# Optimization experiments

Measured on AMD Instinct MI355X. Metric: run time of the kernel, lower is better.

## Reference

```python
import jax, jax.numpy as jnp
import numpy as np

B, T, N, F = 32, 64, 256, 64
TOP_K = 0.2  # ratio of dims to keep per batch element


def setup_inputs() -> dict:
    key = jax.random.key(0)
    ks = jax.random.split(key, 12)
    w = lambda k, shape: jax.random.normal(k, shape, jnp.float32) * 0.05
    z = lambda: jnp.zeros((F,), jnp.float32)
    return {
        "x": jax.random.normal(ks[0], (B, T, N, F), jnp.float32),
        "Wc1": w(ks[1], (3, F, F)), "bc1": z(),
        "Wc2": w(ks[2], (3, F, F)), "bc2": z(),
        "Wc3": w(ks[3], (3, F, F)), "bc3": z(),
        "Wq": w(ks[4], (F, F)), "bq": z(),
        "Wk": w(ks[5], (F, F)), "bk": z(),
        "Wv": w(ks[6], (F, F)), "bv": z(),
        "Wd": w(ks[7], (F, F)), "bd": z(),
        "Wp": w(ks[8], (F, F)), "bp": z(),
    }


def _conv1d(x, W, b, dil):
    # x: [BN, T, F], W: [3, F, F] (WIO), dilated same-padded conv over time
    y = jax.lax.conv_general_dilated(
        x, W, window_strides=(1,), padding="SAME", rhs_dilation=(dil,),
        dimension_numbers=("NWC", "WIO", "NWC"))
    return y + b


@jax.custom_vjp
def ste_round(x):
    return jnp.round(x)

def _ste_fwd(x):
    return jnp.round(x), None

def _ste_bwd(res, g):
    # activation='linear': grad = upstream * 1
    return (g,)

ste_round.defvjp(_ste_fwd, _ste_bwd)


def reference(x, Wc1, bc1, Wc2, bc2, Wc3, bc3, Wq, bq, Wk, bk, Wv, bv, Wd, bd, Wp, bp):
    Bx, Tx, Nx, Fx = x.shape
    # --- dilated conv block over time axis (per node) ---
    xt = jnp.transpose(x, (0, 2, 1, 3)).reshape(Bx * Nx, Tx, Fx)  # [BN,T,F]
    c = jax.nn.relu(_conv1d(xt, Wc1, bc1, 1) + _conv1d(xt, Wc2, bc2, 2)
                    + _conv1d(xt, Wc3, bc3, 3))
    xt = xt + c
    x = jnp.transpose(xt.reshape(Bx, Nx, Tx, Fx), (0, 2, 1, 3))  # [B,T,N,F]
    # --- GAT attention over nodes (faithful: diagonal einsum 'btnn,btnf->btnf') ---
    Q = x @ Wq + bq
    K = x @ Wk + bk
    V = x @ Wv + bv
    scores = jnp.einsum("btnf,btmf->btnm", Q, K) / jnp.sqrt(jnp.float32(Fx))
    A = jax.nn.softmax(scores, axis=-1)
    g = jnp.einsum("btnn,btnf->btnf", A, V)  # diag(A) * V, as in the TF source
    x = x + jax.nn.relu(g)
    # --- dense projection ---
    x = x @ Wd + bd
    # --- inf-norm normalize over last axis, rescale to [0,1] ---
    norm = jnp.max(jnp.abs(x), axis=-1, keepdims=True)
    x = x / norm
    x = 0.5 * (x + 1.0)
    # --- per-batch top-k threshold via full sort ---
    n = Tx * Nx * Fx
    k = int(round(TOP_K * n))  # top_k < 1 => ratio, statically resolved
    ranking = jnp.sort(x.reshape(Bx, -1), axis=-1)  # ascending
    mu = ranking[:, -k - 1].reshape(Bx, 1, 1, 1)
    x = jax.nn.sigmoid(x - mu)
    # --- straight-through binary mask + frozen linear predictor ---
    mask = ste_round(x)
    masked = x * mask
    pred_on_masked = masked @ Wp + bp
    return pred_on_masked, mask
```

## Files before the change

### kernel.cpp

```cpp
#include <hip/hip_runtime.h>
#include <math.h>

#define BB 32
#define TT 64
#define NNODES 256
#define FDIM 64
#define SLICE (NNODES*FDIM)
#define NTOT (BB*TT*NNODES*FDIM)
#define RANK0 838860u

__global__ __launch_bounds__(256) void combine_w(
    const float* __restrict__ Wc1, const float* __restrict__ bc1,
    const float* __restrict__ Wc2, const float* __restrict__ bc2,
    const float* __restrict__ Wc3, const float* __restrict__ bc3,
    float* __restrict__ Wcomb, float* __restrict__ bcomb)
{
  const int FF2 = FDIM*FDIM;
  int gid = blockIdx.x*256 + threadIdx.x;
  if (gid < 7*FF2) {
    int j = gid / FF2, r = gid % FF2;
    float v;
    switch (j) {
      case 0: v = Wc3[r]; break;
      case 1: v = Wc2[r]; break;
      case 2: v = Wc1[r]; break;
      case 3: v = Wc1[FF2+r] + Wc2[FF2+r] + Wc3[FF2+r]; break;
      case 4: v = Wc1[2*FF2+r]; break;
      case 5: v = Wc2[2*FF2+r]; break;
      default: v = Wc3[2*FF2+r]; break;
    }
    Wcomb[gid] = v;
  }
  if (gid < FDIM) bcomb[gid] = bc1[gid] + bc2[gid] + bc3[gid];
}

__global__ __launch_bounds__(256,4) void conv_kernel(
    const float* __restrict__ x, const float* __restrict__ Wcomb,
    const float* __restrict__ bcomb, float* __restrict__ x1)
{
  __shared__ float xs[64*72];
  const int bn = blockIdx.x; const int b = bn >> 8; const int n = bn & 255;
  const int tid = threadIdx.x;
#pragma unroll
  for (int k=0;k<18;k++) xs[k*256+tid] = 0.f;
  __syncthreads();
  const float* xbase = x + ((size_t)b*TT)*SLICE + n*FDIM;
#pragma unroll
  for (int it=0; it<4; it++) {
    int flat4 = it*256 + tid;
    int t = flat4 >> 4, f4 = (flat4 & 15) << 2;
    float4 v = *(const float4*)(xbase + (size_t)t*SLICE + f4);
    xs[(f4+0)*72 + t+4] = v.x;
    xs[(f4+1)*72 + t+4] = v.y;
    xs[(f4+2)*72 + t+4] = v.z;
    xs[(f4+3)*72 + t+4] = v.w;
  }
  __syncthreads();
  const int o = tid & 63;
  const int tb = (tid >> 6) << 4;
  float acc[16];
  const float bco = bcomb[o];
#pragma unroll
  for (int k=0;k<16;k++) acc[k] = bco;
  for (int i=0;i<FDIM;i++) {
    float xr[24];
#pragma unroll
    for (int q=0;q<6;q++) {
      float4 v = *(const float4*)&xs[i*72 + tb + q*4];
      xr[q*4+0]=v.x; xr[q*4+1]=v.y; xr[q*4+2]=v.z; xr[q*4+3]=v.w;
    }
#pragma unroll
    for (int j=0;j<7;j++) {
      float w = Wcomb[(j*FDIM+i)*FDIM + o];
#pragma unroll
      for (int k=0;k<16;k++) acc[k] = fmaf(xr[k+j+1], w, acc[k]);
    }
  }
  float* obase = x1 + ((size_t)b*TT)*SLICE + n*FDIM + o;
#pragma unroll
  for (int k=0;k<16;k++) {
    int t = tb + k;
    float c = acc[k];
    float outv = xs[o*72 + t+4] + (c > 0.f ? c : 0.f);
    obase[(size_t)t*SLICE] = outv;
  }
}

__global__ __launch_bounds__(256,2) void attn_kernel(
    const float* __restrict__ x1,
    const float* __restrict__ Wq, const float* __restrict__ bq,
    const float* __restrict__ Wk, const float* __restrict__ bk,
    const float* __restrict__ Wv, const float* __restrict__ bv,
    const float* __restrict__ Wd, const float* __restrict__ bd,
    float* __restrict__ vout)
{
  __shared__ float ks[NNODES*68];
  const int bt = blockIdx.x;
  const int tid = threadIdx.x;
  const float4* xb4 = (const float4*)(x1 + (size_t)bt*SLICE);
#pragma unroll
  for (int it=0; it<16; it++) {
    int flat4 = it*256 + tid;
    int n = flat4 >> 4, f4 = (flat4 & 15) << 2;
    *(float4*)&ks[n*68 + f4] = xb4[flat4];
  }
  __syncthreads();
  float xr[64];
#pragma unroll
  for (int q=0;q<16;q++) {
    float4 v = *(const float4*)&ks[tid*68 + q*4];
    xr[q*4+0]=v.x; xr[q*4+1]=v.y; xr[q*4+2]=v.z; xr[q*4+3]=v.w;
  }
  {
    float a[64];
#pragma unroll
    for (int o=0;o<64;o++) a[o]=0.f;
    for (int i=0;i<64;i++) {
      float xv = xr[i];
#pragma unroll
      for (int o=0;o<64;o++) a[o] = fmaf(xv, Wk[i*64+o], a[o]);
    }
#pragma unroll
    for (int q=0;q<16;q++) {
      float4 w;
      w.x = a[q*4+0]+bk[q*4+0]; w.y = a[q*4+1]+bk[q*4+1];
      w.z = a[q*4+2]+bk[q*4+2]; w.w = a[q*4+3]+bk[q*4+3];
      *(float4*)&ks[tid*68 + q*4] = w;
    }
  }
  float qr[64];
#pragma unroll
  for (int o=0;o<64;o++) qr[o]=0.f;
  for (int i=0;i<64;i++) {
    float xv = xr[i];
#pragma unroll
    for (int o=0;o<64;o++) qr[o] = fmaf(xv, Wq[i*64+o], qr[o]);
  }
#pragma unroll
  for (int o=0;o<64;o++) qr[o] += bq[o];
  __syncthreads();
  float M = -3.402823466e38f, S = 0.f, diag = 0.f;
  for (int m=0;m<NNODES;m++) {
    float s = 0.f;
#pragma unroll
    for (int q=0;q<16;q++) {
      float4 kv = *(const float4*)&ks[m*68 + q*4];
      s = fmaf(qr[q*4+0], kv.x, s);
      s = fmaf(qr[q*4+1], kv.y, s);
      s = fmaf(qr[q*4+2], kv.z, s);
      s = fmaf(qr[q*4+3], kv.w, s);
    }
    s *= 0.125f;
    if (m == tid) diag = s;
    if (s > M) { S = S * expf(M - s) + 1.f; M = s; }
    else       { S += expf(s - M); }
  }
  const float ann = expf(diag - M) / S;
  float o1[64];
#pragma unroll
  for (int o=0;o<64;o++) o1[o]=0.f;
  for (int i=0;i<64;i++) {
    float xv = xr[i];
#pragma unroll
    for (int o=0;o<64;o++) o1[o] = fmaf(xv, Wv[i*64+o], o1[o]);
  }
#pragma unroll
  for (int o=0;o<64;o++) {
    float g = ann * (o1[o] + bv[o]);
    o1[o] = xr[o] + (g > 0.f ? g : 0.f);
  }
  float dd[64];
#pragma unroll
  for (int o=0;o<64;o++) dd[o]=0.f;
  for (int i=0;i<64;i++) {
    float ov = o1[i];
#pragma unroll
    for (int o=0;o<64;o++) dd[o] = fmaf(ov, Wd[i*64+o], dd[o]);
  }
  float nrm = 0.f;
#pragma unroll
  for (int o=0;o<64;o++) { dd[o] += bd[o]; nrm = fmaxf(nrm, fabsf(dd[o])); }
  __syncthreads();
#pragma unroll
  for (int q=0;q<16;q++) {
    float4 w;
    w.x = 0.5f*(dd[q*4+0]/nrm + 1.f);
    w.y = 0.5f*(dd[q*4+1]/nrm + 1.f);
    w.z = 0.5f*(dd[q*4+2]/nrm + 1.f);
    w.w = 0.5f*(dd[q*4+3]/nrm + 1.f);
    *(float4*)&ks[tid*68 + q*4] = w;
  }
  __syncthreads();
  float4* ob4 = (float4*)(vout + (size_t)bt*SLICE);
#pragma unroll
  for (int it=0;it<16;it++) {
    int flat4 = it*256 + tid;
    int n = flat4 >> 4, f4 = (flat4 & 15) << 2;
    ob4[flat4] = *(const float4*)&ks[n*68 + f4];
  }
}

template<int LEVEL>
__global__ __launch_bounds__(256) void hist_kernel(
    const float* __restrict__ v, unsigned* __restrict__ ghist,
    const unsigned* __restrict__ pfx)
{
  __shared__ unsigned h[4096];
  const int batch = blockIdx.x >> 5, chunk = blockIdx.x & 31;
  const int tid = threadIdx.x;
#pragma unroll
  for (int k=0;k<16;k++) h[k*256+tid] = 0u;
  __syncthreads();
  const unsigned p = pfx ? pfx[batch] : 0u;
  const float4* vb = (const float4*)(v + (size_t)batch*(TT*SLICE)) + chunk*8192 + tid;
  for (int k=0;k<32;k++) {
    float4 q = vb[k*256];
    float e[4] = {q.x,q.y,q.z,q.w};
#pragma unroll
    for (int j=0;j<4;j++) {
      unsigned u = __float_as_uint(e[j]);
      if (LEVEL==1) atomicAdd(&h[u>>20], 1u);
      else if ((u>>20)==p) atomicAdd(&h[(u>>8)&0xFFFu], 1u);
    }
  }
  __syncthreads();
  unsigned* gh = ghist + batch*4096;
#pragma unroll
  for (int k=0;k<16;k++) { unsigned c = h[k*256+tid]; if (c) atomicAdd(&gh[k*256+tid], c); }
}

__global__ __launch_bounds__(256) void hist8_kernel(
    const float* __restrict__ v, unsigned* __restrict__ ghist,
    const unsigned* __restrict__ pfx)
{
  __shared__ unsigned h[256];
  const int batch = blockIdx.x >> 5, chunk = blockIdx.x & 31;
  const int tid = threadIdx.x;
  h[tid] = 0u;
  __syncthreads();
  const unsigned p = pfx[batch];
  const float4* vb = (const float4*)(v + (size_t)batch*(TT*SLICE)) + chunk*8192 + tid;
  for (int k=0;k<32;k++) {
    float4 q = vb[k*256];
    float e[4] = {q.x,q.y,q.z,q.w};
#pragma unroll
    for (int j=0;j<4;j++) {
      unsigned u = __float_as_uint(e[j]);
      if ((u>>8)==p) atomicAdd(&h[u & 255u], 1u);
    }
  }
  __syncthreads();
  unsigned c = h[tid];
  if (c) atomicAdd(&ghist[batch*256+tid], c);
}

template<int PER>
__global__ __launch_bounds__(256) void find_kernel(
    const unsigned* __restrict__ hist,
    const unsigned* __restrict__ rank_in, const unsigned* __restrict__ pfx_in,
    int pfx_shift, unsigned* __restrict__ pfx_out, unsigned* __restrict__ rank_out,
    float* __restrict__ mu, int final_level)
{
  __shared__ unsigned csum[256];
  const int batch = blockIdx.x;
  const int tid = threadIdx.x;
  const unsigned* hb = hist + batch*(PER*256);
  unsigned loc[PER];
  unsigned s = 0;
#pragma unroll
  for (int q=0;q<PER;q++) { loc[q] = hb[tid*PER+q]; s += loc[q]; }
  csum[tid] = s;
  __syncthreads();
  for (int off=1; off<256; off<<=1) {
    unsigned vv = csum[tid];
    unsigned ad = (tid >= off) ? csum[tid-off] : 0u;
    __syncthreads();
    csum[tid] = vv + ad;
    __syncthreads();
  }
  const unsigned rank = rank_in ? rank_in[batch] : RANK0;
  const unsigned excl = csum[tid] - s;
  if (rank >= excl && rank < excl + s) {
    unsigned r = rank - excl;
    int bin = 0;
#pragma unroll
    for (int q=0;q<PER;q++) {
      if (r < loc[q]) { bin = tid*PER + q; break; }
      r -= loc[q];
    }
    unsigned pf = pfx_in ? pfx_in[batch] : 0u;
    unsigned np = (pf << pfx_shift) | (unsigned)bin;
    if (final_level) { mu[batch] = __uint_as_float(np); }
    else { pfx_out[batch] = np; rank_out[batch] = r; }
  }
}

__global__ __launch_bounds__(256,2) void final_kernel(
    const float* __restrict__ v, const float* __restrict__ mu,
    const float* __restrict__ Wp, const float* __restrict__ bp,
    float* __restrict__ pred, float* __restrict__ mask)
{
  __shared__ float sl[NNODES*68];
  const int bt = blockIdx.x;
  const int b = bt >> 6;
  const int tid = threadIdx.x;
  const float4* vb4 = (const float4*)(v + (size_t)bt*SLICE);
#pragma unroll
  for (int it=0; it<16; it++) {
    int flat4 = it*256 + tid;
    int n = flat4 >> 4, f4 = (flat4 & 15) << 2;
    *(float4*)&sl[n*68 + f4] = vb4[flat4];
  }
  __syncthreads();
  const float muv = mu[b];
  float srow[64];
#pragma unroll
  for (int q=0;q<16;q++) {
    float4 vv = *(const float4*)&sl[tid*68 + q*4];
    float e0 = 1.f/(1.f + expf(-(vv.x - muv)));
    float e1 = 1.f/(1.f + expf(-(vv.y - muv)));
    float e2 = 1.f/(1.f + expf(-(vv.z - muv)));
    float e3 = 1.f/(1.f + expf(-(vv.w - muv)));
    float m0 = rintf(e0), m1 = rintf(e1), m2 = rintf(e2), m3 = rintf(e3);
    srow[q*4+0] = e0*m0; srow[q*4+1] = e1*m1; srow[q*4+2] = e2*m2; srow[q*4+3] = e3*m3;
    float4 w; w.x=m0; w.y=m1; w.z=m2; w.w=m3;
    *(float4*)&sl[tid*68 + q*4] = w;
  }
  __syncthreads();
  float4* mb4 = (float4*)(mask + (size_t)bt*SLICE);
#pragma unroll
  for (int it=0; it<16; it++) {
    int flat4 = it*256 + tid;
    int n = flat4 >> 4, f4 = (flat4 & 15) << 2;
    mb4[flat4] = *(const float4*)&sl[n*68 + f4];
  }
  float acc[64];
#pragma unroll
  for (int o=0;o<64;o++) acc[o]=0.f;
  for (int i=0;i<64;i++) {
    float sv = srow[i];
#pragma unroll
    for (int o=0;o<64;o++) acc[o] = fmaf(sv, Wp[i*64+o], acc[o]);
  }
  __syncthreads();
#pragma unroll
  for (int q=0;q<16;q++) {
    float4 w;
    w.x = acc[q*4+0]+bp[q*4+0]; w.y = acc[q*4+1]+bp[q*4+1];
    w.z = acc[q*4+2]+bp[q*4+2]; w.w = acc[q*4+3]+bp[q*4+3];
    *(float4*)&sl[tid*68 + q*4] = w;
  }
  __syncthreads();
  float4* pb4 = (float4*)(pred + (size_t)bt*SLICE);
#pragma unroll
  for (int it=0; it<16; it++) {
    int flat4 = it*256 + tid;
    int n = flat4 >> 4, f4 = (flat4 & 15) << 2;
    pb4[flat4] = *(const float4*)&sl[n*68 + f4];
  }
}

extern "C" void kernel_launch(void* const* d_in, const int* in_sizes, int n_in,
                              void* d_out, int out_size, void* d_ws, size_t ws_size,
                              hipStream_t stream) {
  const float* x   = (const float*)d_in[0];
  const float* Wc1 = (const float*)d_in[1];  const float* bc1 = (const float*)d_in[2];
  const float* Wc2 = (const float*)d_in[3];  const float* bc2 = (const float*)d_in[4];
  const float* Wc3 = (const float*)d_in[5];  const float* bc3 = (const float*)d_in[6];
  const float* Wq  = (const float*)d_in[7];  const float* bq  = (const float*)d_in[8];
  const float* Wk  = (const float*)d_in[9];  const float* bk  = (const float*)d_in[10];
  const float* Wv  = (const float*)d_in[11]; const float* bv  = (const float*)d_in[12];
  const float* Wd  = (const float*)d_in[13]; const float* bd  = (const float*)d_in[14];
  const float* Wp  = (const float*)d_in[15]; const float* bp  = (const float*)d_in[16];

  float* pred = (float*)d_out;
  float* mask = pred + NTOT;

  unsigned* hist1 = (unsigned*)d_ws;
  unsigned* hist2 = hist1 + 32*4096;
  unsigned* hist3 = hist2 + 32*4096;
  unsigned* pfx1  = hist3 + 32*256;
  unsigned* rank1 = pfx1 + 32;
  unsigned* pfx2  = rank1 + 32;
  unsigned* rank2 = pfx2 + 32;
  float*    muv   = (float*)(rank2 + 32);
  float*    Wcomb = muv + 32;
  float*    bcomb = Wcomb + 7*64*64;

  hipMemsetAsync(d_ws, 0, (size_t)(32*4096*2 + 32*256)*sizeof(unsigned), stream);
  combine_w<<<112, 256, 0, stream>>>(Wc1,bc1,Wc2,bc2,Wc3,bc3,Wcomb,bcomb);
  conv_kernel<<<BB*NNODES, 256, 0, stream>>>(x, Wcomb, bcomb, mask );
  attn_kernel<<<BB*TT, 256, 0, stream>>>(mask , Wq,bq,Wk,bk,Wv,bv,Wd,bd, pred );
  hist_kernel<1><<<1024, 256, 0, stream>>>(pred, hist1, nullptr);
  find_kernel<16><<<32, 256, 0, stream>>>(hist1, nullptr, nullptr, 0, pfx1, rank1, nullptr, 0);
  hist_kernel<2><<<1024, 256, 0, stream>>>(pred, hist2, pfx1);
  find_kernel<16><<<32, 256, 0, stream>>>(hist2, rank1, pfx1, 12, pfx2, rank2, nullptr, 0);
  hist8_kernel<<<1024, 256, 0, stream>>>(pred, hist3, pfx2);
  find_kernel<1><<<32, 256, 0, stream>>>(hist3, rank2, pfx2, 8, nullptr, nullptr, muv, 1);
  final_kernel<<<BB*TT, 256, 0, stream>>>(pred , muv, Wp, bp, pred, mask);
}
```

Measured before the change: 1.491 ms.

## Fold Q/K projections into combined Wq·Wkᵀ bilinear form with packed FMAs

```diff
diff --git a/kernel.cpp b/kernel.cpp
--- a/kernel.cpp
+++ b/kernel.cpp
@@ -8,6 +8,15 @@
 #define SLICE (NNODES*FDIM)
 #define NTOT (BB*TT*NNODES*FDIM)
 #define RANK0 838860u
+
+typedef float v2f __attribute__((ext_vector_type(2)));
+__device__ __forceinline__ v2f pkfma(v2f a, v2f b, v2f c) {
+#if __has_builtin(__builtin_elementwise_fma)
+  return __builtin_elementwise_fma(a, b, c);
+#else
+  v2f r; r.x = fmaf(a.x,b.x,c.x); r.y = fmaf(a.y,b.y,c.y); return r;
+#endif
+}
 
 __global__ __launch_bounds__(256) void combine_w(
     const float* __restrict__ Wc1, const float* __restrict__ bc1,
@@ -34,6 +43,35 @@
   if (gid < FDIM) bcomb[gid] = bc1[gid] + bc2[gid] + bc3[gid];
 }
 
+__global__ __launch_bounds__(256) void combine_qk(
+    const float* __restrict__ Wq, const float* __restrict__ bq,
+    const float* __restrict__ Wk, const float* __restrict__ bk,
+    float* __restrict__ Wqk, float* __restrict__ zb,
+    float* __restrict__ wqbk, float* __restrict__ bqbk)
+{
+  int gid = blockIdx.x*256 + threadIdx.x;
+  if (gid < 4096) {
+    int i = gid >> 6, j = gid & 63;
+    float a = 0.f;
+    for (int o=0;o<64;o++) a = fmaf(Wq[i*64+o], Wk[j*64+o], a);
+    Wqk[i*64+j] = a;
+  } else if (gid < 4160) {
+    int j = gid - 4096;
+    float a = 0.f;
+    for (int o=0;o<64;o++) a = fmaf(bq[o], Wk[j*64+o], a);
+    zb[j] = a;
+  } else if (gid < 4224) {
+    int i = gid - 4160;
+    float a = 0.f;
+    for (int o=0;o<64;o++) a = fmaf(Wq[i*64+o], bk[o], a);
+    wqbk[i] = a;
+  } else if (gid == 4224) {
+    float a = 0.f;
+    for (int o=0;o<64;o++) a = fmaf(bq[o], bk[o], a);
+    bqbk[0] = a;
+  }
+}
+
 __global__ __launch_bounds__(256,4) void conv_kernel(
     const float* __restrict__ x, const float* __restrict__ Wcomb,
     const float* __restrict__ bcomb, float* __restrict__ x1)
@@ -88,8 +126,8 @@
 
 __global__ __launch_bounds__(256,2) void attn_kernel(
     const float* __restrict__ x1,
-    const float* __restrict__ Wq, const float* __restrict__ bq,
-    const float* __restrict__ Wk, const float* __restrict__ bk,
+    const float* __restrict__ Wqk, const float* __restrict__ zb,
+    const float* __restrict__ wqbk, const float* __restrict__ bqbk,
     const float* __restrict__ Wv, const float* __restrict__ bv,
     const float* __restrict__ Wd, const float* __restrict__ bd,
     float* __restrict__ vout)
@@ -105,81 +143,110 @@
     *(float4*)&ks[n*68 + f4] = xb4[flat4];
   }
   __syncthreads();
-  float xr[64];
-#pragma unroll
-  for (int q=0;q<16;q++) {
-    float4 v = *(const float4*)&ks[tid*68 + q*4];
-    xr[q*4+0]=v.x; xr[q*4+1]=v.y; xr[q*4+2]=v.z; xr[q*4+3]=v.w;
-  }
+
+  v2f zp[32];
+  float d = bqbk[0];
   {
-    float a[64];
-#pragma unroll
-    for (int o=0;o<64;o++) a[o]=0.f;
+    float xr[64];
+#pragma unroll
+    for (int q=0;q<16;q++) {
+      float4 v = *(const float4*)&ks[tid*68 + q*4];
+      xr[q*4+0]=v.x; xr[q*4+1]=v.y; xr[q*4+2]=v.z; xr[q*4+3]=v.w;
+    }
+#pragma unroll
+    for (int j=0;j<32;j++) { v2f t; t.x = zb[2*j]; t.y = zb[2*j+1]; zp[j] = t; }
     for (int i=0;i<64;i++) {
-      float xv = xr[i];
-#pragma unroll
-      for (int o=0;o<64;o++) a[o] = fmaf(xv, Wk[i*64+o], a[o]);
-    }
+      v2f xv; xv.x = xr[i]; xv.y = xr[i];
+      const float4* wr = (const float4*)(Wqk + i*64);
+#pragma unroll
+      for (int q=0;q<16;q++) {
+        float4 w4 = wr[q];
+        v2f wlo; wlo.x=w4.x; wlo.y=w4.y;
+        v2f whi; whi.x=w4.z; whi.y=w4.w;
+        zp[2*q]   = pkfma(xv, wlo, zp[2*q]);
+        zp[2*q+1] = pkfma(xv, whi, zp[2*q+1]);
+      }
+      d = fmaf(xr[i], wqbk[i], d);
+    }
+  }
+
+  float S0 = 0.f, S1 = 0.f, diag = 0.f;
+  for (int m=0;m<NNODES;m+=2) {
+    v2f a0={0.f,0.f}, a1={0.f,0.f}, b0={0.f,0.f}, b1={0.f,0.f};
 #pragma unroll
     for (int q=0;q<16;q++) {
-      float4 w;
-      w.x = a[q*4+0]+bk[q*4+0]; w.y = a[q*4+1]+bk[q*4+1];
-      w.z = a[q*4+2]+bk[q*4+2]; w.w = a[q*4+3]+bk[q*4+3];
-      *(float4*)&ks[tid*68 + q*4] = w;
-    }
-  }
-  float qr[64];
-#pragma unroll
-  for (int o=0;o<64;o++) qr[o]=0.f;
-  for (int i=0;i<64;i++) {
-    float xv = xr[i];
-#pragma unroll
-    for (int o=0;o<64;o++) qr[o] = fmaf(xv, Wq[i*64+o], qr[o]);
-  }
-#pragma unroll
-  for (int o=0;o<64;o++) qr[o] += bq[o];
-  __syncthreads();
-  float M = -3.402823466e38f, S = 0.f, diag = 0.f;
-  for (int m=0;m<NNODES;m++) {
-    float s = 0.f;
+      float4 k0 = *(const float4*)&ks[m*68 + q*4];
+      float4 k1 = *(const float4*)&ks[(m+1)*68 + q*4];
+      v2f k0lo; k0lo.x=k0.x; k0lo.y=k0.y;
+      v2f k0hi; k0hi.x=k0.z; k0hi.y=k0.w;
+      v2f k1lo; k1lo.x=k1.x; k1lo.y=k1.y;
+      v2f k1hi; k1hi.x=k1.z; k1hi.y=k1.w;
+      a0 = pkfma(zp[2*q],   k0lo, a0);
+      a1 = pkfma(zp[2*q+1], k0hi, a1);
+      b0 = pkfma(zp[2*q],   k1lo, b0);
+      b1 = pkfma(zp[2*q+1], k1hi, b1);
+    }
+    float s0 = (((a0.x+a0.y)+(a1.x+a1.y)) + d)*0.125f;
+    float s1 = (((b0.x+b0.y)+(b1.x+b1.y)) + d)*0.125f;
+    if (tid == m)   diag = s0;
+    if (tid == m+1) diag = s1;
+    S0 += __expf(s0);
+    S1 += __expf(s1);
+  }
+  const float ann = __expf(diag) / (S0 + S1);
+
+  float o1[64];
+  {
+    float xr[64];
 #pragma unroll
     for (int q=0;q<16;q++) {
-      float4 kv = *(const float4*)&ks[m*68 + q*4];
-      s = fmaf(qr[q*4+0], kv.x, s);
-      s = fmaf(qr[q*4+1], kv.y, s);
-      s = fmaf(qr[q*4+2], kv.z, s);
-      s = fmaf(qr[q*4+3], kv.w, s);
-    }
-    s *= 0.125f;
-    if (m == tid) diag = s;
-    if (s > M) { S = S * expf(M - s) + 1.f; M = s; }
-    else       { S += expf(s - M); }
-  }
-  const float ann = expf(diag - M) / S;
-  float o1[64];
-#pragma unroll
-  for (int o=0;o<64;o++) o1[o]=0.f;
-  for (int i=0;i<64;i++) {
-    float xv = xr[i];
-#pragma unroll
-    for (int o=0;o<64;o++) o1[o] = fmaf(xv, Wv[i*64+o], o1[o]);
-  }
-#pragma unroll
-  for (int o=0;o<64;o++) {
-    float g = ann * (o1[o] + bv[o]);
-    o1[o] = xr[o] + (g > 0.f ? g : 0.f);
+      float4 v = *(const float4*)&ks[tid*68 + q*4];
+      xr[q*4+0]=v.x; xr[q*4+1]=v.y; xr[q*4+2]=v.z; xr[q*4+3]=v.w;
+    }
+    v2f vacc[32];
+#pragma unroll
+    for (int j=0;j<32;j++) { v2f t; t.x = bv[2*j]; t.y = bv[2*j+1]; vacc[j] = t; }
+    for (int i=0;i<64;i++) {
+      v2f xv; xv.x = xr[i]; xv.y = xr[i];
+      const float4* wr = (const float4*)(Wv + i*64);
+#pragma unroll
+      for (int q=0;q<16;q++) {
+        float4 w4 = wr[q];
+        v2f wlo; wlo.x=w4.x; wlo.y=w4.y;
+        v2f whi; whi.x=w4.z; whi.y=w4.w;
+        vacc[2*q]   = pkfma(xv, wlo, vacc[2*q]);
+        vacc[2*q+1] = pkfma(xv, whi, vacc[2*q+1]);
+      }
+    }
+#pragma unroll
+    for (int o=0;o<64;o++) {
+      float g = ann * ((o & 1) ? vacc[o>>1].y : vacc[o>>1].x);
+      o1[o] = xr[o] + (g > 0.f ? g : 0.f);
+    }
   }
   float dd[64];
-#pragma unroll
-  for (int o=0;o<64;o++) dd[o]=0.f;
-  for (int i=0;i<64;i++) {
-    float ov = o1[i];
-#pragma unroll
-    for (int o=0;o<64;o++) dd[o] = fmaf(ov, Wd[i*64+o], dd[o]);
+  {
+    v2f dacc[32];
+#pragma unroll
+    for (int j=0;j<32;j++) { v2f t; t.x = bd[2*j]; t.y = bd[2*j+1]; dacc[j] = t; }
+    for (int i=0;i<64;i++) {
+      v2f xv; xv.x = o1[i]; xv.y = o1[i];
+      const float4* wr = (const float4*)(Wd + i*64);
+#pragma unroll
+      for (int q=0;q<16;q++) {
+        float4 w4 = wr[q];
+        v2f wlo; wlo.x=w4.x; wlo.y=w4.y;
+        v2f whi; whi.x=w4.z; whi.y=w4.w;
+        dacc[2*q]   = pkfma(xv, wlo, dacc[2*q]);
+        dacc[2*q+1] = pkfma(xv, whi, dacc[2*q+1]);
+      }
+    }
+#pragma unroll
+    for (int o=0;o<64;o++) dd[o] = (o & 1) ? dacc[o>>1].y : dacc[o>>1].x;
   }
   float nrm = 0.f;
 #pragma unroll
-  for (int o=0;o<64;o++) { dd[o] += bd[o]; nrm = fmaxf(nrm, fabsf(dd[o])); }
+  for (int o=0;o<64;o++) nrm = fmaxf(nrm, fabsf(dd[o]));
   __syncthreads();
 #pragma unroll
   for (int q=0;q<16;q++) {
@@ -386,11 +453,16 @@
   float*    muv   = (float*)(rank2 + 32);
   float*    Wcomb = muv + 32;
   float*    bcomb = Wcomb + 7*64*64;
+  float*    Wqk   = bcomb + 64;
+  float*    zbv   = Wqk + 64*64;
+  float*    wqbk  = zbv + 64;
+  float*    bqbk  = wqbk + 64;
 
   hipMemsetAsync(d_ws, 0, (size_t)(32*4096*2 + 32*256)*sizeof(unsigned), stream);
   combine_w<<<112, 256, 0, stream>>>(Wc1,bc1,Wc2,bc2,Wc3,bc3,Wcomb,bcomb);
+  combine_qk<<<17, 256, 0, stream>>>(Wq,bq,Wk,bk,Wqk,zbv,wqbk,bqbk);
   conv_kernel<<<BB*NNODES, 256, 0, stream>>>(x, Wcomb, bcomb, mask );
-  attn_kernel<<<BB*TT, 256, 0, stream>>>(mask , Wq,bq,Wk,bk,Wv,bv,Wd,bd, pred );
+  attn_kernel<<<BB*TT, 256, 0, stream>>>(mask , Wqk,zbv,wqbk,bqbk, Wv,bv,Wd,bd, pred );
   hist_kernel<1><<<1024, 256, 0, stream>>>(pred, hist1, nullptr);
   find_kernel<16><<<32, 256, 0, stream>>>(hist1, nullptr, nullptr, 0, pfx1, rank1, nullptr, 0);
   hist_kernel<2><<<1024, 256, 0, stream>>>(pred, hist2, pfx1);
```

New measurement: 1.196 ms. -19.8%, faster.
